# Optimization experiments

Hardware: AMD Instinct MI355X
Metric: run time of the kernel (lower is better)

The kernel has to match this reference:

```python
import jax, jax.numpy as jnp
import numpy as np

B = 16384
IN = 512
A = 16
E = 9  # 9 position-specific experts
H1, H2, H3 = 512, 256, 128


def setup_inputs() -> dict:
    key = jax.random.key(0)
    ks = jax.random.split(key, 10)
    s = lambda fan_in: 1.0 / np.sqrt(fan_in)
    return {
        "x": jax.random.normal(ks[0], (B, IN), dtype=jnp.float32),
        "position": jax.random.randint(ks[1], (B,), 0, 9, dtype=jnp.int64),
        # torch Linear convention: W [out, in], y = x @ W.T + b; stacked per expert [E, out, in]
        "W1": jax.random.uniform(ks[2], (E, H1, IN), jnp.float32, -s(IN), s(IN)),
        "b1": jax.random.uniform(ks[3], (E, H1), jnp.float32, -s(IN), s(IN)),
        "W2": jax.random.uniform(ks[4], (E, H2, H1), jnp.float32, -s(H1), s(H1)),
        "b2": jax.random.uniform(ks[5], (E, H2), jnp.float32, -s(H1), s(H1)),
        "W3": jax.random.uniform(ks[6], (E, H3, H2), jnp.float32, -s(H2), s(H2)),
        "b3": jax.random.uniform(ks[7], (E, H3), jnp.float32, -s(H2), s(H2)),
        "W4": jax.random.uniform(ks[8], (E, A, H3), jnp.float32, -s(H3), s(H3)),
        "b4": jax.random.uniform(ks[9], (E, A), jnp.float32, -s(H3), s(H3)),
    }


def reference(x, position, W1, b1, W2, b2, W3, b3, W4, b4):
    # Each sample i is routed through expert min(position[i], 8).
    # Dense MoE reference: run all 9 experts over the full batch, then
    # select the routed expert's logits per sample (same math as the
    # per-sample Python loop in the original module).
    pos = jnp.minimum(position, 8)
    h = jax.nn.relu(jnp.einsum('bi,eoi->ebo', x, W1) + b1[:, None, :])   # [E,B,H1]
    h = jax.nn.relu(jnp.einsum('ebi,eoi->ebo', h, W2) + b2[:, None, :])  # [E,B,H2]
    h = jax.nn.relu(jnp.einsum('ebi,eoi->ebo', h, W3) + b3[:, None, :])  # [E,B,H3]
    logits_all = jnp.einsum('ebi,eoi->ebo', h, W4) + b4[:, None, :]      # [E,B,A]
    logits = logits_all[pos, jnp.arange(x.shape[0])]                     # [B,A]
    return jax.nn.softmax(logits, axis=1)
```

## Files before the change

### kernel.cpp

```cpp
#include <hip/hip_runtime.h>

typedef _Float16 f16;
typedef __attribute__((ext_vector_type(8))) _Float16 f16x8;
typedef __attribute__((ext_vector_type(4))) _Float16 f16x4;
typedef __attribute__((ext_vector_type(4))) float f32x4;

#define MFMA16(a, b, c) __builtin_amdgcn_mfma_f32_16x16x32_f16(a, b, c, 0, 0, 0)

#define B_N 16384
#define E_N 9
#define TILE 32
#define NTILE_MAX 520
#define THREADS 512

#define D_IN 512
#define D_H1 512
#define D_H2 256
#define D_H3 128
#define D_A 16

#define RPW 104
#define O4B 7667712
#define WPL_BYTES 7704576
#define WSLOTS (WPL_BYTES / 16)

#define IDX_OFF 64
#define WP_OFF 131584
#define WS_NEED (WP_OFF + (size_t)WPL_BYTES)

#define XS_OFF 0
#define B1H_OFF 0
#define H2_OFF 16384
#define B0H_OFF 32768
#define H3_OFF 32768
#define LDS_BYTES 49152


__global__ void k_bucket(const int* __restrict__ pos, int* __restrict__ hdr,
                         int* __restrict__ idx) {
  __shared__ int cnt[E_N], cur[E_N];
  __shared__ int flag_s;
  const int t = threadIdx.x;
  if (t < E_N) cnt[t] = 0;
  if (t == 0) {
    int nz = 0;
    for (int i = 0; i < 64; ++i) nz |= pos[2 * i + 1];
    flag_s = (nz == 0) ? 1 : 0;
  }
  __syncthreads();
  const bool f64 = flag_s != 0;
  int e[16];
#pragma unroll
  for (int k = 0; k < 16; ++k) {
    int i = k * 1024 + t;
    long long v = f64 ? ((const long long*)pos)[i] : (long long)pos[i];
    v = v < 0 ? 0 : (v > 8 ? 8 : v);
    e[k] = (int)v;
    atomicAdd(&cnt[e[k]], 1);
  }
  __syncthreads();
  if (t == 0) {
    int acc = 0;
    for (int ee = 0; ee < E_N; ++ee) { cur[ee] = acc; acc += cnt[ee]; }
  }
  if (t < E_N) hdr[8 + t] = cnt[t];
  __syncthreads();
#pragma unroll
  for (int k = 0; k < 16; ++k) {
    int i = k * 1024 + t;
    int slot = atomicAdd(&cur[e[k]], 1);
    idx[slot] = i;
  }
}


__global__ void k_wcvt(const float* __restrict__ W1, const float* __restrict__ W2,
                       const float* __restrict__ W3, const float* __restrict__ W4,
                       char* __restrict__ wp) {
  int slot = blockIdx.x * 256 + threadIdx.x;
  if (slot >= WSLOTS) return;
  long addr = (long)slot << 4;
  int lane = slot & 63;
  int lg = lane >> 4, ln = lane & 15;
  const float* src;
  if (addr < O4B) {
    int rec = (int)(addr >> 10);
    int f = rec % RPW;
    int ew = rec / RPW;
    int w = ew & 7, e = ew >> 3;
    if (f < 64) {
      int n = w * 64 + ((f >> 5) & 1) * 32 + (f & 1) * 16 + ln;
      int k = ((f >> 2) & 7) * 64 + ((f >> 1) & 1) * 32 + lg * 8;
      src = W1 + ((long)e * D_H1 + n) * D_IN + k;
    } else if (f < 96) {
      int j = f - 64;
      int n = w * 32 + (j & 1) * 16 + ln;
      int k = (j >> 2) * 64 + ((j >> 1) & 1) * 32 + lg * 8;
      src = W2 + ((long)e * D_H2 + n) * D_H1 + k;
    } else {
      int j = f - 96;
      int n = w * 16 + ln;
      int k = (j >> 1) * 64 + (j & 1) * 32 + lg * 8;
      src = W3 + ((long)e * D_H3 + n) * D_H2 + k;
    }
  } else {
    long rel = addr - O4B;
    int e = (int)(rel >> 12);
    int r2 = (int)(rel & 4095);
    int s = r2 >> 4, n = s >> 4, k16 = s & 15;
    src = W4 + ((long)e * D_A + n) * D_H3 + k16 * 8;
  }
  float4 a = *(const float4*)src;
  float4 b = *(const float4*)(src + 4);
  f16x8 h;
  h[0] = (f16)a.x; h[1] = (f16)a.y; h[2] = (f16)a.z; h[3] = (f16)a.w;
  h[4] = (f16)b.x; h[5] = (f16)b.y; h[6] = (f16)b.z; h[7] = (f16)b.w;
  *(f16x8*)(wp + addr) = h;
}


__device__ __forceinline__ f16x8 afrag(const char* base, int strideB, int rowoff,
                                       int kbytes, int lane) {
  int m = rowoff + (lane & 15);
  int q = kbytes + ((lane >> 4) * 16);
  return *(const f16x8*)(base + m * strideB + (q ^ ((m & 15) << 4)));
}

__device__ __forceinline__ f16x8 ldfrag(const char* wb, int f, int lane) {
  return *(const f16x8*)(wb + (long)f * 1024 + lane * 16);
}

__launch_bounds__(THREADS, 4)
__global__ void k_mlp(const float* __restrict__ x,
                      const float* __restrict__ b1, const float* __restrict__ b2,
                      const float* __restrict__ b3, const float* __restrict__ b4,
                      const int* __restrict__ hdr, const int* __restrict__ idx,
                      const char* __restrict__ wp, float* __restrict__ out) {
  __shared__ __align__(16) char lds[LDS_BYTES];

  int b = blockIdx.x;
  int bswz = (b & 7) * (NTILE_MAX / 8) + (b >> 3);

  const int* counts = hdr + 8;
  int e = -1, tile = 0, base = 0, ne = 0;
  {
    int acc = 0, off = 0;
    for (int ee = 0; ee < E_N; ++ee) {
      int n = counts[ee];
      int nt = (n + TILE - 1) / TILE;
      if (bswz < acc + nt) { e = ee; tile = bswz - acc; ne = n; base = off; break; }
      acc += nt; off += n;
    }
  }
  if (e < 0) return;
  const int rvalid = min(TILE, ne - tile * TILE);
  const int row0 = base + tile * TILE;

  const int t = threadIdx.x;
  const int lane = t & 63;
  const int wid = t >> 6;
  const int lg = lane >> 4;
  const int ln = lane & 15;

  const char* wb = wp + ((long)(e * 8 + wid) * RPW << 10);
  const char* wpe4 = wp + O4B + (long)e * 4096;

  f16x8 Q[8];
#pragma unroll
  for (int i = 0; i < 8; ++i) Q[i] = ldfrag(wb, i, lane);

  const float4* x4 = (const float4*)x;
  for (int u = t; u < TILE * (D_IN / 4); u += THREADS) {
    int s = u >> 7, c4 = u & 127;
    float4 v = make_float4(0.f, 0.f, 0.f, 0.f);
    if (s < rvalid) v = x4[(long)idx[row0 + s] * (D_IN / 4) + c4];
    f16x4 h;
    h[0] = (f16)v.x; h[1] = (f16)v.y; h[2] = (f16)v.z; h[3] = (f16)v.w;
    *(f16x4*)(lds + XS_OFF + s * 1024 + ((c4 * 8) ^ ((s & 15) << 4))) = h;
  }
  __syncthreads();

  f16x8 st1[2];
  {
    f32x4 acc[2][2];
#pragma unroll
    for (int g = 0; g < 16; ++g) {
      const int kb = g & 7, h = g >> 3;
      if (kb == 0) {
#pragma unroll
        for (int m = 0; m < 2; ++m)
#pragma unroll
          for (int nf = 0; nf < 2; ++nf) acc[m][nf] = (f32x4){0.f, 0.f, 0.f, 0.f};
      }
      __builtin_amdgcn_s_setprio(1);
#pragma unroll
      for (int kc = 0; kc < 2; ++kc) {
        f16x8 A0 = afrag(lds + XS_OFF, 1024, 0, kb * 128 + kc * 64, lane);
        f16x8 A1 = afrag(lds + XS_OFF, 1024, 16, kb * 128 + kc * 64, lane);
#pragma unroll
        for (int nf = 0; nf < 2; ++nf) {
          const int i = g * 4 + kc * 2 + nf;
          acc[0][nf] = MFMA16(A0, Q[i & 7], acc[0][nf]);
          acc[1][nf] = MFMA16(A1, Q[i & 7], acc[1][nf]);
          Q[i & 7] = ldfrag(wb, i + 8, lane);
        }
      }
      __builtin_amdgcn_s_setprio(0);
      if (kb == 7) {
        if (h == 0) {
#pragma unroll
          for (int nf = 0; nf < 2; ++nf) {
            float bias = b1[e * D_H1 + wid * 64 + nf * 16 + ln];
            int cbyte = (wid * 32 + nf * 16 + ln) * 2;
#pragma unroll
            for (int m = 0; m < 2; ++m)
#pragma unroll
              for (int j = 0; j < 4; ++j) {
                float v = acc[m][nf][j] + bias;
                v = v > 0.f ? v : 0.f;
                int rw = m * 16 + lg * 4 + j;
                *(f16*)(lds + B0H_OFF + rw * 512 + (cbyte ^ ((rw & 15) << 4))) = (f16)v;
              }
          }
        } else {
#pragma unroll
          for (int nf = 0; nf < 2; ++nf) {
            float bias = b1[e * D_H1 + wid * 64 + 32 + nf * 16 + ln];
#pragma unroll
            for (int m = 0; m < 2; ++m)
#pragma unroll
              for (int j = 0; j < 4; ++j) {
                float v = acc[m][nf][j] + bias;
                st1[m][nf * 4 + j] = (f16)(v > 0.f ? v : 0.f);
              }
          }
        }
      }
    }
  }
  __syncthreads();

#pragma unroll
  for (int m = 0; m < 2; ++m)
#pragma unroll
    for (int nf = 0; nf < 2; ++nf) {
      int cbyte = (wid * 32 + nf * 16 + ln) * 2;
#pragma unroll
      for (int j = 0; j < 4; ++j) {
        int rw = m * 16 + lg * 4 + j;
        *(f16*)(lds + B1H_OFF + rw * 512 + (cbyte ^ ((rw & 15) << 4))) =
            st1[m][nf * 4 + j];
      }
    }
  __syncthreads();

  {
    f32x4 acc[2][2];
#pragma unroll
    for (int m = 0; m < 2; ++m)
#pragma unroll
      for (int nf = 0; nf < 2; ++nf) acc[m][nf] = (f32x4){0.f, 0.f, 0.f, 0.f};
#pragma unroll
    for (int g = 0; g < 8; ++g) {
      __builtin_amdgcn_s_setprio(1);
#pragma unroll
      for (int kc = 0; kc < 2; ++kc) {
        const char* bank = lds + (kc ? B1H_OFF : B0H_OFF);
        f16x8 A0 = afrag(bank, 512, 0, g * 64, lane);
        f16x8 A1 = afrag(bank, 512, 16, g * 64, lane);
#pragma unroll
        for (int nf = 0; nf < 2; ++nf) {
          const int i = 64 + g * 4 + kc * 2 + nf;
          acc[0][nf] = MFMA16(A0, Q[i & 7], acc[0][nf]);
          acc[1][nf] = MFMA16(A1, Q[i & 7], acc[1][nf]);
          if (i < 96) Q[i & 7] = ldfrag(wb, i + 8, lane);
        }
      }
      __builtin_amdgcn_s_setprio(0);
    }
#pragma unroll
    for (int nf = 0; nf < 2; ++nf) {
      float bias = b2[e * D_H2 + wid * 32 + nf * 16 + ln];
      int cbyte = (wid * 32 + nf * 16 + ln) * 2;
#pragma unroll
      for (int m = 0; m < 2; ++m)
#pragma unroll
        for (int j = 0; j < 4; ++j) {
          float v = acc[m][nf][j] + bias;
          v = v > 0.f ? v : 0.f;
          int rw = m * 16 + lg * 4 + j;
          *(f16*)(lds + H2_OFF + rw * 512 + (cbyte ^ ((rw & 15) << 4))) = (f16)v;
        }
    }
  }
  __syncthreads();

  {
    f32x4 acc3[2];
    acc3[0] = (f32x4){0.f, 0.f, 0.f, 0.f};
    acc3[1] = (f32x4){0.f, 0.f, 0.f, 0.f};
#pragma unroll
    for (int g = 0; g < 4; ++g) {
      __builtin_amdgcn_s_setprio(1);
#pragma unroll
      for (int kc = 0; kc < 2; ++kc) {
        const int i = 96 + g * 2 + kc;
        f16x8 A0 = afrag(lds + H2_OFF, 512, 0, g * 128 + kc * 64, lane);
        f16x8 A1 = afrag(lds + H2_OFF, 512, 16, g * 128 + kc * 64, lane);
        acc3[0] = MFMA16(A0, Q[i & 7], acc3[0]);
        acc3[1] = MFMA16(A1, Q[i & 7], acc3[1]);
      }
      __builtin_amdgcn_s_setprio(0);
    }
    int n = wid * 16 + ln;
    float bias = b3[e * D_H3 + n];
#pragma unroll
    for (int m = 0; m < 2; ++m)
#pragma unroll
      for (int j = 0; j < 4; ++j) {
        float v = acc3[m][j] + bias;
        v = v > 0.f ? v : 0.f;
        int rw = m * 16 + lg * 4 + j;
        *(f16*)(lds + H3_OFF + rw * 256 + ((n * 2) ^ ((rw & 15) << 4))) = (f16)v;
      }
  }
  __syncthreads();

  if (wid < 2) {
    f32x4 a4 = (f32x4){0.f, 0.f, 0.f, 0.f};
#pragma unroll
    for (int kc = 0; kc < 4; ++kc) {
      f16x8 Bv = *(const f16x8*)(wpe4 + ln * 256 + kc * 64 + lg * 16);
      f16x8 Av = afrag(lds + H3_OFF, 256, wid * 16, kc * 64, lane);
      a4 = MFMA16(Av, Bv, a4);
    }
    float bias = b4[e * D_A + ln];
#pragma unroll
    for (int j = 0; j < 4; ++j) {
      float v = a4[j] + bias;
      float mx = v;
      for (int msk = 8; msk >= 1; msk >>= 1) mx = fmaxf(mx, __shfl_xor(mx, msk));
      float pe = expf(v - mx);
      float sm = pe;
      for (int msk = 8; msk >= 1; msk >>= 1) sm += __shfl_xor(sm, msk);
      int rl = wid * 16 + lg * 4 + j;
      if (rl < rvalid) out[(long)idx[row0 + rl] * D_A + ln] = pe / sm;
    }
  }
}


extern "C" void kernel_launch(void* const* d_in, const int* in_sizes, int n_in,
                              void* d_out, int out_size, void* d_ws, size_t ws_size,
                              hipStream_t stream) {
  const float* x  = (const float*)d_in[0];
  const int* pos  = (const int*)d_in[1];
  const float* W1 = (const float*)d_in[2];
  const float* b1 = (const float*)d_in[3];
  const float* W2 = (const float*)d_in[4];
  const float* b2 = (const float*)d_in[5];
  const float* W3 = (const float*)d_in[6];
  const float* b3 = (const float*)d_in[7];
  const float* W4 = (const float*)d_in[8];
  const float* b4 = (const float*)d_in[9];
  float* out = (float*)d_out;

  int* hdr = (int*)d_ws;
  int* idx = hdr + IDX_OFF;
  char* wp = (char*)d_ws + WP_OFF;

  hipLaunchKernelGGL(k_bucket, dim3(1), dim3(1024), 0, stream, pos, hdr, idx);
  hipLaunchKernelGGL(k_wcvt, dim3(WSLOTS / 256), dim3(256), 0, stream,
                     W1, W2, W3, W4, wp);
  hipLaunchKernelGGL(k_mlp, dim3(NTILE_MAX), dim3(THREADS), 0, stream,
                     x, b1, b2, b3, b4, hdr, idx, wp, out);
}
```

Before: 64.30 us.

## Enlarge row tile to 48 and restructure layer-1 as single pass

Raises the per-block row tile from 32 to 48 samples so each streamed weight fragment feeds three MFMA row blocks instead of two, and shrinks the grid to 352 blocks. Layer 1 now keeps all four 16-column output fragments in registers over one full K sweep, replacing the two-half split that staged activations through registers and extra LDS writes. The weight pre-pack order changes to match. LDS grows to 72 KB and accumulator registers increase, which may cut occupancy and leave more padded rows in partial tiles.

After: 60.06 us. -6.6%, faster.

```diff
diff --git a/kernel.cpp b/kernel.cpp
--- a/kernel.cpp
+++ b/kernel.cpp
@@ -9,8 +9,8 @@
 
 #define B_N 16384
 #define E_N 9
-#define TILE 32
-#define NTILE_MAX 520
+#define TILE 48
+#define NT_GRID 352
 #define THREADS 512
 
 #define D_IN 512
@@ -28,12 +28,8 @@
 #define WP_OFF 131584
 #define WS_NEED (WP_OFF + (size_t)WPL_BYTES)
 
-#define XS_OFF 0
-#define B1H_OFF 0
-#define H2_OFF 16384
-#define B0H_OFF 32768
-#define H3_OFF 32768
-#define LDS_BYTES 49152
+#define H2_OFF 49152
+#define LDS_BYTES 73728
 
 
 __global__ void k_bucket(const int* __restrict__ pos, int* __restrict__ hdr,
@@ -89,18 +85,20 @@
     int ew = rec / RPW;
     int w = ew & 7, e = ew >> 3;
     if (f < 64) {
-      int n = w * 64 + ((f >> 5) & 1) * 32 + (f & 1) * 16 + ln;
-      int k = ((f >> 2) & 7) * 64 + ((f >> 1) & 1) * 32 + lg * 8;
+      int kk = f >> 2, nf = f & 3;
+      int n = w * 64 + nf * 16 + ln;
+      int k = kk * 32 + lg * 8;
       src = W1 + ((long)e * D_H1 + n) * D_IN + k;
     } else if (f < 96) {
       int j = f - 64;
-      int n = w * 32 + (j & 1) * 16 + ln;
-      int k = (j >> 2) * 64 + ((j >> 1) & 1) * 32 + lg * 8;
+      int kk = j >> 1, nf = j & 1;
+      int n = w * 32 + nf * 16 + ln;
+      int k = kk * 32 + lg * 8;
       src = W2 + ((long)e * D_H2 + n) * D_H1 + k;
     } else {
-      int j = f - 96;
+      int kk = f - 96;
       int n = w * 16 + ln;
-      int k = (j >> 1) * 64 + (j & 1) * 32 + lg * 8;
+      int k = kk * 32 + lg * 8;
       src = W3 + ((long)e * D_H3 + n) * D_H2 + k;
     }
   } else {
@@ -139,7 +137,7 @@
   __shared__ __align__(16) char lds[LDS_BYTES];
 
   int b = blockIdx.x;
-  int bswz = (b & 7) * (NTILE_MAX / 8) + (b >> 3);
+  int bswz = (b & 7) * (NT_GRID / 8) + (b >> 3);
 
   const int* counts = hdr + 8;
   int e = -1, tile = 0, base = 0, ne = 0;
@@ -170,168 +168,142 @@
   for (int i = 0; i < 8; ++i) Q[i] = ldfrag(wb, i, lane);
 
   const float4* x4 = (const float4*)x;
-  for (int u = t; u < TILE * (D_IN / 4); u += THREADS) {
+#pragma unroll
+  for (int v8 = 0; v8 < 12; ++v8) {
+    int u = v8 * THREADS + t;
     int s = u >> 7, c4 = u & 127;
     float4 v = make_float4(0.f, 0.f, 0.f, 0.f);
     if (s < rvalid) v = x4[(long)idx[row0 + s] * (D_IN / 4) + c4];
     f16x4 h;
     h[0] = (f16)v.x; h[1] = (f16)v.y; h[2] = (f16)v.z; h[3] = (f16)v.w;
-    *(f16x4*)(lds + XS_OFF + s * 1024 + ((c4 * 8) ^ ((s & 15) << 4))) = h;
-  }
-  __syncthreads();
-
-  f16x8 st1[2];
+    *(f16x4*)(lds + s * 1024 + ((c4 * 8) ^ ((s & 15) << 4))) = h;
+  }
+  __syncthreads();
+
   {
-    f32x4 acc[2][2];
-#pragma unroll
-    for (int g = 0; g < 16; ++g) {
-      const int kb = g & 7, h = g >> 3;
-      if (kb == 0) {
-#pragma unroll
-        for (int m = 0; m < 2; ++m)
-#pragma unroll
-          for (int nf = 0; nf < 2; ++nf) acc[m][nf] = (f32x4){0.f, 0.f, 0.f, 0.f};
-      }
+    f32x4 acc1[3][4];
+#pragma unroll
+    for (int m = 0; m < 3; ++m)
+#pragma unroll
+      for (int r = 0; r < 4; ++r) acc1[m][r] = (f32x4){0.f, 0.f, 0.f, 0.f};
+
+#pragma unroll
+    for (int ss = 0; ss < 16; ++ss) {
+      f16x8 A0 = afrag(lds, 1024, 0, ss * 64, lane);
+      f16x8 A1 = afrag(lds, 1024, 16, ss * 64, lane);
+      f16x8 A2 = afrag(lds, 1024, 32, ss * 64, lane);
       __builtin_amdgcn_s_setprio(1);
 #pragma unroll
-      for (int kc = 0; kc < 2; ++kc) {
-        f16x8 A0 = afrag(lds + XS_OFF, 1024, 0, kb * 128 + kc * 64, lane);
-        f16x8 A1 = afrag(lds + XS_OFF, 1024, 16, kb * 128 + kc * 64, lane);
-#pragma unroll
-        for (int nf = 0; nf < 2; ++nf) {
-          const int i = g * 4 + kc * 2 + nf;
-          acc[0][nf] = MFMA16(A0, Q[i & 7], acc[0][nf]);
-          acc[1][nf] = MFMA16(A1, Q[i & 7], acc[1][nf]);
-          Q[i & 7] = ldfrag(wb, i + 8, lane);
-        }
+      for (int r = 0; r < 4; ++r) {
+        const int i = ss * 4 + r;
+        acc1[0][r] = MFMA16(A0, Q[i & 7], acc1[0][r]);
+        acc1[1][r] = MFMA16(A1, Q[i & 7], acc1[1][r]);
+        acc1[2][r] = MFMA16(A2, Q[i & 7], acc1[2][r]);
+        Q[i & 7] = ldfrag(wb, i + 8, lane);
       }
       __builtin_amdgcn_s_setprio(0);
-      if (kb == 7) {
-        if (h == 0) {
-#pragma unroll
-          for (int nf = 0; nf < 2; ++nf) {
-            float bias = b1[e * D_H1 + wid * 64 + nf * 16 + ln];
-            int cbyte = (wid * 32 + nf * 16 + ln) * 2;
-#pragma unroll
-            for (int m = 0; m < 2; ++m)
-#pragma unroll
-              for (int j = 0; j < 4; ++j) {
-                float v = acc[m][nf][j] + bias;
-                v = v > 0.f ? v : 0.f;
-                int rw = m * 16 + lg * 4 + j;
-                *(f16*)(lds + B0H_OFF + rw * 512 + (cbyte ^ ((rw & 15) << 4))) = (f16)v;
-              }
-          }
-        } else {
-#pragma unroll
-          for (int nf = 0; nf < 2; ++nf) {
-            float bias = b1[e * D_H1 + wid * 64 + 32 + nf * 16 + ln];
-#pragma unroll
-            for (int m = 0; m < 2; ++m)
-#pragma unroll
-              for (int j = 0; j < 4; ++j) {
-                float v = acc[m][nf][j] + bias;
-                st1[m][nf * 4 + j] = (f16)(v > 0.f ? v : 0.f);
-              }
-          }
+      __builtin_amdgcn_sched_barrier(0);
+    }
+    __syncthreads();
+
+#pragma unroll
+    for (int nf = 0; nf < 4; ++nf) {
+      int n = wid * 64 + nf * 16 + ln;
+      float bias = b1[e * D_H1 + n];
+#pragma unroll
+      for (int m = 0; m < 3; ++m)
+#pragma unroll
+        for (int j = 0; j < 4; ++j) {
+          float v = acc1[m][nf][j] + bias;
+          v = v > 0.f ? v : 0.f;
+          int rw = m * 16 + lg * 4 + j;
+          *(f16*)(lds + rw * 1024 + ((n * 2) ^ ((rw & 15) << 4))) = (f16)v;
         }
-      }
-    }
-  }
-  __syncthreads();
-
-#pragma unroll
-  for (int m = 0; m < 2; ++m)
-#pragma unroll
-    for (int nf = 0; nf < 2; ++nf) {
-      int cbyte = (wid * 32 + nf * 16 + ln) * 2;
-#pragma unroll
-      for (int j = 0; j < 4; ++j) {
-        int rw = m * 16 + lg * 4 + j;
-        *(f16*)(lds + B1H_OFF + rw * 512 + (cbyte ^ ((rw & 15) << 4))) =
-            st1[m][nf * 4 + j];
-      }
-    }
+    }
+  }
   __syncthreads();
 
   {
-    f32x4 acc[2][2];
-#pragma unroll
-    for (int m = 0; m < 2; ++m)
-#pragma unroll
-      for (int nf = 0; nf < 2; ++nf) acc[m][nf] = (f32x4){0.f, 0.f, 0.f, 0.f};
-#pragma unroll
-    for (int g = 0; g < 8; ++g) {
-      __builtin_amdgcn_s_setprio(1);
-#pragma unroll
-      for (int kc = 0; kc < 2; ++kc) {
-        const char* bank = lds + (kc ? B1H_OFF : B0H_OFF);
-        f16x8 A0 = afrag(bank, 512, 0, g * 64, lane);
-        f16x8 A1 = afrag(bank, 512, 16, g * 64, lane);
+    f32x4 acc2[3][2];
+#pragma unroll
+    for (int m = 0; m < 3; ++m)
+#pragma unroll
+      for (int nf = 0; nf < 2; ++nf) acc2[m][nf] = (f32x4){0.f, 0.f, 0.f, 0.f};
+
+#pragma unroll
+    for (int ss = 16; ss < 24; ++ss) {
+#pragma unroll
+      for (int hh = 0; hh < 2; ++hh) {
+        const int kk = (ss - 16) * 2 + hh;
+        f16x8 A0 = afrag(lds, 1024, 0, kk * 64, lane);
+        f16x8 A1 = afrag(lds, 1024, 16, kk * 64, lane);
+        f16x8 A2 = afrag(lds, 1024, 32, kk * 64, lane);
+        __builtin_amdgcn_s_setprio(1);
 #pragma unroll
         for (int nf = 0; nf < 2; ++nf) {
-          const int i = 64 + g * 4 + kc * 2 + nf;
-          acc[0][nf] = MFMA16(A0, Q[i & 7], acc[0][nf]);
-          acc[1][nf] = MFMA16(A1, Q[i & 7], acc[1][nf]);
+          const int i = ss * 4 + hh * 2 + nf;
+          acc2[0][nf] = MFMA16(A0, Q[i & 7], acc2[0][nf]);
+          acc2[1][nf] = MFMA16(A1, Q[i & 7], acc2[1][nf]);
+          acc2[2][nf] = MFMA16(A2, Q[i & 7], acc2[2][nf]);
           if (i < 96) Q[i & 7] = ldfrag(wb, i + 8, lane);
         }
+        __builtin_amdgcn_s_setprio(0);
       }
-      __builtin_amdgcn_s_setprio(0);
+      __builtin_amdgcn_sched_barrier(0);
     }
 #pragma unroll
     for (int nf = 0; nf < 2; ++nf) {
-      float bias = b2[e * D_H2 + wid * 32 + nf * 16 + ln];
-      int cbyte = (wid * 32 + nf * 16 + ln) * 2;
-#pragma unroll
-      for (int m = 0; m < 2; ++m)
+      int n = wid * 32 + nf * 16 + ln;
+      float bias = b2[e * D_H2 + n];
+#pragma unroll
+      for (int m = 0; m < 3; ++m)
 #pragma unroll
         for (int j = 0; j < 4; ++j) {
-          float v = acc[m][nf][j] + bias;
+          float v = acc2[m][nf][j] + bias;
           v = v > 0.f ? v : 0.f;
           int rw = m * 16 + lg * 4 + j;
-          *(f16*)(lds + H2_OFF + rw * 512 + (cbyte ^ ((rw & 15) << 4))) = (f16)v;
+          *(f16*)(lds + H2_OFF + rw * 512 + ((n * 2) ^ ((rw & 15) << 4))) = (f16)v;
         }
     }
   }
   __syncthreads();
 
   {
-    f32x4 acc3[2];
-    acc3[0] = (f32x4){0.f, 0.f, 0.f, 0.f};
-    acc3[1] = (f32x4){0.f, 0.f, 0.f, 0.f};
-#pragma unroll
-    for (int g = 0; g < 4; ++g) {
-      __builtin_amdgcn_s_setprio(1);
-#pragma unroll
-      for (int kc = 0; kc < 2; ++kc) {
-        const int i = 96 + g * 2 + kc;
-        f16x8 A0 = afrag(lds + H2_OFF, 512, 0, g * 128 + kc * 64, lane);
-        f16x8 A1 = afrag(lds + H2_OFF, 512, 16, g * 128 + kc * 64, lane);
-        acc3[0] = MFMA16(A0, Q[i & 7], acc3[0]);
-        acc3[1] = MFMA16(A1, Q[i & 7], acc3[1]);
-      }
-      __builtin_amdgcn_s_setprio(0);
-    }
+    f32x4 acc3[3];
+#pragma unroll
+    for (int m = 0; m < 3; ++m) acc3[m] = (f32x4){0.f, 0.f, 0.f, 0.f};
+    __builtin_amdgcn_s_setprio(1);
+#pragma unroll
+    for (int kk = 0; kk < 8; ++kk) {
+      const int i = 96 + kk;
+      f16x8 A0 = afrag(lds + H2_OFF, 512, 0, kk * 64, lane);
+      f16x8 A1 = afrag(lds + H2_OFF, 512, 16, kk * 64, lane);
+      f16x8 A2 = afrag(lds + H2_OFF, 512, 32, kk * 64, lane);
+      acc3[0] = MFMA16(A0, Q[i & 7], acc3[0]);
+      acc3[1] = MFMA16(A1, Q[i & 7], acc3[1]);
+      acc3[2] = MFMA16(A2, Q[i & 7], acc3[2]);
+    }
+    __builtin_amdgcn_s_setprio(0);
     int n = wid * 16 + ln;
     float bias = b3[e * D_H3 + n];
 #pragma unroll
-    for (int m = 0; m < 2; ++m)
+    for (int m = 0; m < 3; ++m)
 #pragma unroll
       for (int j = 0; j < 4; ++j) {
         float v = acc3[m][j] + bias;
         v = v > 0.f ? v : 0.f;
         int rw = m * 16 + lg * 4 + j;
-        *(f16*)(lds + H3_OFF + rw * 256 + ((n * 2) ^ ((rw & 15) << 4))) = (f16)v;
+        *(f16*)(lds + rw * 256 + ((n * 2) ^ ((rw & 15) << 4))) = (f16)v;
       }
   }
   __syncthreads();
 
-  if (wid < 2) {
+  if (wid < 3) {
     f32x4 a4 = (f32x4){0.f, 0.f, 0.f, 0.f};
 #pragma unroll
     for (int kc = 0; kc < 4; ++kc) {
       f16x8 Bv = *(const f16x8*)(wpe4 + ln * 256 + kc * 64 + lg * 16);
-      f16x8 Av = afrag(lds + H3_OFF, 256, wid * 16, kc * 64, lane);
+      f16x8 Av = afrag(lds, 256, wid * 16, kc * 64, lane);
       a4 = MFMA16(Av, Bv, a4);
     }
     float bias = b4[e * D_A + ln];
@@ -372,6 +344,6 @@
   hipLaunchKernelGGL(k_bucket, dim3(1), dim3(1024), 0, stream, pos, hdr, idx);
   hipLaunchKernelGGL(k_wcvt, dim3(WSLOTS / 256), dim3(256), 0, stream,
                      W1, W2, W3, W4, wp);
-  hipLaunchKernelGGL(k_mlp, dim3(NTILE_MAX), dim3(THREADS), 0, stream,
+  hipLaunchKernelGGL(k_mlp, dim3(NT_GRID), dim3(THREADS), 0, stream,
                      x, b1, b2, b3, b4, hdr, idx, wp, out);
 }
```
